# Performance work log

Hardware: AMD Instinct MI355X
Metric: run time of the kernel (lower is better)

The kernel has to match this reference:

```python
import jax, jax.numpy as jnp
import numpy as np

T, B_SZ = 1024, 1024
NX, NU, ND, NM, NDT, NH = 128, 64, 32, 32, 32, 128


def setup_inputs() -> dict:
    key = jax.random.key(0)
    ks = jax.random.split(key, 10)
    return {
        "x": jax.random.normal(ks[0], (B_SZ, NX), jnp.float32),
        "M_flow": jax.random.normal(ks[1], (T, B_SZ, NM), jnp.float32),
        "DT": jax.random.normal(ks[2], (T, B_SZ, NDT), jnp.float32),
        "D": jax.random.normal(ks[3], (T, B_SZ, ND), jnp.float32),
        # ConstrainedLinear(nx, nx): weight and scalar init with torch.rand -> uniform[0,1)
        "A_weight": jax.random.uniform(ks[4], (NX, NX), jnp.float32),
        "A_scalar": jax.random.uniform(ks[5], (NX, NX), jnp.float32),
        # nn.Linear(in, out, bias=False) weights are [out, in]
        "B_w": jax.random.normal(ks[6], (NX, NU), jnp.float32) * (1.0 / np.sqrt(NU)),
        "E_w": jax.random.normal(ks[7], (NX, ND), jnp.float32) * (1.0 / np.sqrt(ND)),
        "hf1_w": jax.random.normal(ks[8], (NH, NM + NDT), jnp.float32) * (1.0 / np.sqrt(NM + NDT)),
        "hf2_w": jax.random.normal(ks[9], (NU, NH), jnp.float32) * (1.0 / np.sqrt(NH)),
    }


def reference(x, M_flow, DT, D, A_weight, A_scalar, B_w, E_w, hf1_w, hf2_w):
    # Constrained weight: ((1 - 0.1*sigmoid(scalar)) * softmax(weight, dim=1)).T
    # It is constant across time, so compute once (torch redundantly recomputes it per step).
    s_clamped = 1.0 - 0.1 * jax.nn.sigmoid(A_scalar)
    W_eff = (s_clamped * jax.nn.softmax(A_weight, axis=1)).T  # [nx, nx]

    # Per-step control input u_t depends only on exogenous M_flow/DT -> vectorize over time.
    md = jnp.concatenate([M_flow, DT], axis=2)                # [T, B, n_m+n_dT]
    h = jax.nn.relu(jnp.einsum('tbi,hi->tbh', md, hf1_w))     # [T, B, n_hidden]
    u = jax.nn.relu(jnp.einsum('tbh,uh->tbu', h, hf2_w))      # [T, B, nu]

    # Precompute additive drive B(u_t) + E(d_t); only x@W_eff is sequential.
    drive = jnp.einsum('tbu,xu->tbx', u, B_w) + jnp.einsum('tbd,xd->tbx', D, E_w)

    def step(x_prev, drive_t):
        x_new = x_prev @ W_eff + drive_t
        return x_new, x_new

    _, X = jax.lax.scan(step, x, drive)  # X: [T, B, nx]
    Y = X[:, :, -1]                      # [T, B]
    return X, Y
```

## Files before the change

kernel.cpp:

```cpp
#include <hip/hip_runtime.h>

typedef _Float16 h4 __attribute__((ext_vector_type(4)));
typedef _Float16 h8 __attribute__((ext_vector_type(8)));
typedef float f4 __attribute__((ext_vector_type(4)));

#define MFMA16(a, b, c) __builtin_amdgcn_mfma_f32_16x16x32_f16((a), (b), (c), 0, 0, 0)

static constexpr int TT  = 1024;
static constexpr int BS  = 1024;
static constexpr int LCH = 64;
static constexpr int NCH = 16;
static constexpr size_t XTOT = (size_t)TT * BS * 128;

static constexpr size_t WS_WT16 = 0;
static constexpr size_t WS_HF1  = 32768;
static constexpr size_t WS_HF2  = 49152;
static constexpr size_t WS_BW   = 65536;
static constexpr size_t WS_EW   = 81920;
static constexpr size_t WS_W32A = 122880;
static constexpr size_t WS_W32B = 188416;
static constexpr size_t WS_F    = 253952;
static constexpr size_t WS_INIT = WS_F + (size_t)NCH * BS * 128 * 4;
static constexpr size_t WS_DRV  = WS_INIT + (size_t)NCH * BS * 128 * 4;

__global__ void prep_kernel(const float* __restrict__ Aw, const float* __restrict__ As,
                            const float* __restrict__ hf1, const float* __restrict__ hf2,
                            const float* __restrict__ Bw, const float* __restrict__ Ew,
                            char* __restrict__ ws)
{
    const int tid = threadIdx.x;
    const int bid = blockIdx.x;
    if (bid < 128) {
        __shared__ float red[128];
        const int n = bid;
        const float a = Aw[n * 128 + tid];
        red[tid] = a;
        __syncthreads();
        for (int s = 64; s > 0; s >>= 1) {
            if (tid < s) red[tid] = fmaxf(red[tid], red[tid + s]);
            __syncthreads();
        }
        const float mx = red[0];
        __syncthreads();
        const float e = expf(a - mx);
        red[tid] = e;
        __syncthreads();
        for (int s = 64; s > 0; s >>= 1) {
            if (tid < s) red[tid] += red[tid + s];
            __syncthreads();
        }
        const float sm  = e / red[0];
        const float asv = As[n * 128 + tid];
        const float sc  = 1.0f - 0.1f * (1.0f / (1.0f + expf(-asv)));
        const float val = sc * sm;
        ((_Float16*)(ws + WS_WT16))[n * 128 + tid] = (_Float16)val;
        ((float*)(ws + WS_W32A))[n * 128 + tid]    = val;
    } else {
        const int b2 = bid - 128;
        for (int i = b2 * 128 + tid; i < 8192; i += 32 * 128) {
            ((_Float16*)(ws + WS_HF1))[i] = (_Float16)hf1[i];
            ((_Float16*)(ws + WS_HF2))[i] = (_Float16)hf2[i];
            ((_Float16*)(ws + WS_BW))[i]  = (_Float16)Bw[i];
            if (i < 4096) ((_Float16*)(ws + WS_EW))[i] = (_Float16)Ew[i];
        }
    }
}

__global__ void matsq_kernel(const float* __restrict__ in, float* __restrict__ out)
{
    const int idx = blockIdx.x * 256 + threadIdx.x;
    const int n = idx >> 7, k = idx & 127;
    float acc = 0.f;
    for (int m = 0; m < 128; ++m) acc += in[m * 128 + k] * in[n * 128 + m];
    out[idx] = acc;
}

__global__ __launch_bounds__(256, 3)
void drive_kernel(const float* __restrict__ Mfl, const float* __restrict__ DTi,
                  const float* __restrict__ Din, char* __restrict__ ws)
{
    const int tid  = threadIdx.x;
    const int lane = tid & 63;
    const int w    = tid >> 6;
    const int cl   = lane & 15;
    const int gq   = lane >> 4;
    const int bt   = blockIdx.x & 63;
    const int tq   = blockIdx.x >> 6;
    const int b0   = bt * 16;

    const _Float16* Hf1  = (const _Float16*)(ws + WS_HF1);
    const _Float16* Hf2  = (const _Float16*)(ws + WS_HF2);
    const _Float16* Bw16 = (const _Float16*)(ws + WS_BW);
    const _Float16* Ew16 = (const _Float16*)(ws + WS_EW);
    _Float16* Drv        = (_Float16*)(ws + WS_DRV);

    __shared__ __align__(16) _Float16 mds[4][16 * 64];
    __shared__ __align__(16) _Float16 dts[4][16 * 32];
    __shared__ __align__(16) _Float16 hs[4][16 * 128];
    __shared__ __align__(16) _Float16 us[4][16 * 64];

    h8 hf1f[2][2], bwf[2][2], ewf[2], hf2f[4];
#pragma unroll
    for (int nt = 0; nt < 2; ++nt) {
        const int ng = w * 32 + nt * 16 + cl;
#pragma unroll
        for (int kk = 0; kk < 2; ++kk) {
            hf1f[nt][kk] = *(const h8*)&Hf1[ng * 64 + kk * 32 + gq * 8];
            bwf[nt][kk]  = *(const h8*)&Bw16[ng * 64 + kk * 32 + gq * 8];
        }
        ewf[nt] = *(const h8*)&Ew16[ng * 32 + gq * 8];
    }
    {
        const int ng = w * 16 + cl;
#pragma unroll
        for (int kk = 0; kk < 4; ++kk)
            hf2f[kk] = *(const h8*)&Hf2[ng * 128 + kk * 32 + gq * 8];
    }

    const int qrow = (tid & 127) >> 3;
    const int qc4  = (tid & 7) * 4;
    f4 pm[4], pd[4];
#pragma unroll
    for (int s = 0; s < 4; ++s) {
        const size_t t  = (size_t)tq * 4 + s;
        const size_t rb = (t * BS + b0 + qrow) * 32 + qc4;
        pm[s] = (tid < 128) ? *(const f4*)&Mfl[rb] : *(const f4*)&DTi[rb];
        if (tid < 128) pd[s] = *(const f4*)&Din[rb];
    }
#pragma unroll
    for (int s = 0; s < 4; ++s) {
        const int col = (tid < 128) ? qc4 : (32 + qc4);
        h4 hv;
#pragma unroll
        for (int j = 0; j < 4; ++j) hv[j] = (_Float16)pm[s][j];
        *(h4*)&mds[s][qrow * 64 + (((col >> 3) ^ (qrow & 7)) * 8) + (col & 7)] = hv;
        if (tid < 128) {
            h4 h2;
#pragma unroll
            for (int j = 0; j < 4; ++j) h2[j] = (_Float16)pd[s][j];
            *(h4*)&dts[s][qrow * 32 + (((qc4 >> 3) ^ (qrow & 3)) * 8) + (qc4 & 7)] = h2;
        }
    }
    __syncthreads();

#pragma unroll
    for (int s = 0; s < 4; ++s) {
        f4 ha[2] = {};
#pragma unroll
        for (int kk = 0; kk < 2; ++kk) {
            h8 a = *(const h8*)&mds[s][cl * 64 + (((kk * 4 + gq) ^ (cl & 7)) * 8)];
            ha[0] = MFMA16(a, hf1f[0][kk], ha[0]);
            ha[1] = MFMA16(a, hf1f[1][kk], ha[1]);
        }
#pragma unroll
        for (int nt = 0; nt < 2; ++nt) {
            const int colg = w * 32 + nt * 16 + cl;
#pragma unroll
            for (int r = 0; r < 4; ++r) {
                const int row = gq * 4 + r;
                hs[s][row * 128 + (((colg >> 3) ^ (row & 15)) * 8) + (colg & 7)] =
                    (_Float16)fmaxf(ha[nt][r], 0.f);
            }
        }
    }
    __syncthreads();

#pragma unroll
    for (int s = 0; s < 4; ++s) {
        f4 ua = {};
#pragma unroll
        for (int kk = 0; kk < 4; ++kk) {
            h8 a = *(const h8*)&hs[s][cl * 128 + (((kk * 4 + gq) ^ (cl & 15)) * 8)];
            ua = MFMA16(a, hf2f[kk], ua);
        }
        const int colg = w * 16 + cl;
#pragma unroll
        for (int r = 0; r < 4; ++r) {
            const int row = gq * 4 + r;
            us[s][row * 64 + (((colg >> 3) ^ (row & 7)) * 8) + (colg & 7)] =
                (_Float16)fmaxf(ua[r], 0.f);
        }
    }
    __syncthreads();

#pragma unroll
    for (int s = 0; s < 4; ++s) {
        f4 acc[2] = {};
#pragma unroll
        for (int kk = 0; kk < 2; ++kk) {
            h8 a = *(const h8*)&us[s][cl * 64 + (((kk * 4 + gq) ^ (cl & 7)) * 8)];
            acc[0] = MFMA16(a, bwf[0][kk], acc[0]);
            acc[1] = MFMA16(a, bwf[1][kk], acc[1]);
        }
        {
            h8 a = *(const h8*)&dts[s][cl * 32 + ((gq ^ (cl & 3)) * 8)];
            acc[0] = MFMA16(a, ewf[0], acc[0]);
            acc[1] = MFMA16(a, ewf[1], acc[1]);
        }
        h8 hv;
#pragma unroll
        for (int nt = 0; nt < 2; ++nt)
#pragma unroll
            for (int r = 0; r < 4; ++r) hv[nt * 4 + r] = (_Float16)acc[nt][r];
        const size_t t = (size_t)tq * 4 + s;
        *(h8*)&Drv[((t * 64 + bt) * 256 + tid) * 8] = hv;
    }
}

template <bool FINAL>
__global__ __launch_bounds__(256, 4)
void scan_kernel(char* __restrict__ ws, float* __restrict__ Xout, float* __restrict__ Yout)
{
    const int tid  = threadIdx.x;
    const int lane = tid & 63;
    const int w    = tid >> 6;
    const int cl   = lane & 15;
    const int gq   = lane >> 4;
    const int bt   = blockIdx.x & 63;
    const int c    = blockIdx.x >> 6;
    const int b0   = bt * 16;

    const _Float16* Wt16 = (const _Float16*)(ws + WS_WT16);
    const _Float16* Drv  = (const _Float16*)(ws + WS_DRV);
    float* Fbuf          = (float*)(ws + WS_F);
    const float* Init    = (const float*)(ws + WS_INIT);

    __shared__ __align__(16) _Float16 xs[2][16 * 128];

    h8 wtf[2][4];
#pragma unroll
    for (int nt = 0; nt < 2; ++nt) {
        const int ng = w * 32 + nt * 16 + cl;
#pragma unroll
        for (int kk = 0; kk < 4; ++kk)
            wtf[nt][kk] = *(const h8*)&Wt16[ng * 128 + kk * 32 + gq * 8];
    }

    if constexpr (FINAL) {
        const int row = tid >> 4, c8 = tid & 15;
        const float* src = &Init[((size_t)c * BS + b0 + row) * 128 + c8 * 8];
        f4 v0 = *(const f4*)src;
        f4 v1 = *(const f4*)(src + 4);
        h8 hv;
#pragma unroll
        for (int j = 0; j < 4; ++j) { hv[j] = (_Float16)v0[j]; hv[4 + j] = (_Float16)v1[j]; }
        *(h8*)&xs[0][row * 128 + ((c8 ^ row) & 15) * 8] = hv;
    } else {
        h8 z = {};
        *(h8*)&xs[0][tid * 8] = z;
    }
    __syncthreads();

    const size_t dbase = (((size_t)c * 64) * 64 + bt) * 2048 + (size_t)tid * 8;
    h8 dc = *(const h8*)&Drv[dbase];

    int cur = 0;
    for (int k = 0; k < LCH; ++k) {
        f4 acc[2];
#pragma unroll
        for (int nt = 0; nt < 2; ++nt)
#pragma unroll
            for (int r = 0; r < 4; ++r) acc[nt][r] = (float)dc[nt * 4 + r];

        if (k + 1 < LCH) dc = *(const h8*)&Drv[dbase + (size_t)(k + 1) * 64 * 2048];

#pragma unroll
        for (int kk = 0; kk < 4; ++kk) {
            h8 a = *(const h8*)&xs[cur][cl * 128 + (((kk * 4 + gq) ^ (cl & 15)) * 8)];
            acc[0] = MFMA16(a, wtf[0][kk], acc[0]);
            acc[1] = MFMA16(a, wtf[1][kk], acc[1]);
        }

        const int nxt = cur ^ 1;
        if constexpr (FINAL) {
            const size_t t = (size_t)c * LCH + k;
#pragma unroll
            for (int nt = 0; nt < 2; ++nt) {
                const int colg = w * 32 + nt * 16 + cl;
#pragma unroll
                for (int r = 0; r < 4; ++r) {
                    const int row = gq * 4 + r;
                    const float v = acc[nt][r];
                    Xout[(t * BS + b0 + row) * 128 + colg] = v;
                    xs[nxt][row * 128 + (((colg >> 3) ^ (row & 15)) * 8) + (colg & 7)] =
                        (_Float16)v;
                }
            }
            if (w == 3 && cl == 15) {
#pragma unroll
                for (int r = 0; r < 4; ++r)
                    Yout[t * BS + b0 + gq * 4 + r] = acc[1][r];
            }
        } else {
            if (k == LCH - 1) {
#pragma unroll
                for (int nt = 0; nt < 2; ++nt) {
                    const int colg = w * 32 + nt * 16 + cl;
#pragma unroll
                    for (int r = 0; r < 4; ++r) {
                        const int row = gq * 4 + r;
                        Fbuf[((size_t)c * BS + b0 + row) * 128 + colg] = acc[nt][r];
                    }
                }
            } else {
#pragma unroll
                for (int nt = 0; nt < 2; ++nt) {
                    const int colg = w * 32 + nt * 16 + cl;
#pragma unroll
                    for (int r = 0; r < 4; ++r) {
                        const int row = gq * 4 + r;
                        xs[nxt][row * 128 + (((colg >> 3) ^ (row & 15)) * 8) + (colg & 7)] =
                            (_Float16)acc[nt][r];
                    }
                }
            }
        }
        __syncthreads();
        cur = nxt;
    }
}

__global__ __launch_bounds__(256, 2)
void carry_kernel(const float* __restrict__ x_in, char* __restrict__ ws)
{
    const int tid  = threadIdx.x;
    const int lane = tid & 63;
    const int w    = tid >> 6;
    const int cl   = lane & 15;
    const int gq   = lane >> 4;
    const int b0   = blockIdx.x * 16;

    const float* WL32 = (const float*)(ws + WS_W32A);
    const float* Fbuf = (const float*)(ws + WS_F);
    float* Init       = (float*)(ws + WS_INIT);

    __shared__ __align__(16) _Float16 xs[2][16 * 128];

    h8 wlf[2][4];
#pragma unroll
    for (int nt = 0; nt < 2; ++nt) {
        const int ng = w * 32 + nt * 16 + cl;
#pragma unroll
        for (int kk = 0; kk < 4; ++kk) {
            f4 a0 = *(const f4*)&WL32[ng * 128 + kk * 32 + gq * 8];
            f4 a1 = *(const f4*)&WL32[ng * 128 + kk * 32 + gq * 8 + 4];
#pragma unroll
            for (int j = 0; j < 4; ++j) {
                wlf[nt][kk][j]     = (_Float16)a0[j];
                wlf[nt][kk][4 + j] = (_Float16)a1[j];
            }
        }
    }

    {
        const int row = tid >> 4, c8 = tid & 15;
        const float* src = &x_in[(b0 + row) * 128 + c8 * 8];
        f4 v0 = *(const f4*)src, v1 = *(const f4*)(src + 4);
        float* dst = &Init[((size_t)(b0 + row)) * 128 + c8 * 8];
        *(f4*)dst = v0;
        *(f4*)(dst + 4) = v1;
        h8 hv;
#pragma unroll
        for (int j = 0; j < 4; ++j) { hv[j] = (_Float16)v0[j]; hv[4 + j] = (_Float16)v1[j]; }
        *(h8*)&xs[0][row * 128 + ((c8 ^ row) & 15) * 8] = hv;
    }
    __syncthreads();

    int cur = 0;
    for (int cc = 1; cc < NCH; ++cc) {
        f4 acc[2] = {};
#pragma unroll
        for (int kk = 0; kk < 4; ++kk) {
            h8 a = *(const h8*)&xs[cur][cl * 128 + (((kk * 4 + gq) ^ (cl & 15)) * 8)];
            acc[0] = MFMA16(a, wlf[0][kk], acc[0]);
            acc[1] = MFMA16(a, wlf[1][kk], acc[1]);
        }
        const int nxt = cur ^ 1;
#pragma unroll
        for (int nt = 0; nt < 2; ++nt) {
            const int colg = w * 32 + nt * 16 + cl;
#pragma unroll
            for (int r = 0; r < 4; ++r) {
                const int row = gq * 4 + r;
                const float v =
                    acc[nt][r] + Fbuf[((size_t)(cc - 1) * BS + b0 + row) * 128 + colg];
                Init[((size_t)cc * BS + b0 + row) * 128 + colg] = v;
                xs[nxt][row * 128 + (((colg >> 3) ^ (row & 15)) * 8) + (colg & 7)] =
                    (_Float16)v;
            }
        }
        __syncthreads();
        cur = nxt;
    }
}

extern "C" void kernel_launch(void* const* d_in, const int* in_sizes, int n_in,
                              void* d_out, int out_size, void* d_ws, size_t ws_size,
                              hipStream_t stream)
{
    const float* x_in = (const float*)d_in[0];
    const float* Mfl  = (const float*)d_in[1];
    const float* DTi  = (const float*)d_in[2];
    const float* Din  = (const float*)d_in[3];
    const float* Aw   = (const float*)d_in[4];
    const float* As   = (const float*)d_in[5];
    const float* Bw   = (const float*)d_in[6];
    const float* Ew   = (const float*)d_in[7];
    const float* hf1  = (const float*)d_in[8];
    const float* hf2  = (const float*)d_in[9];
    char* ws    = (char*)d_ws;
    float* Xout = (float*)d_out;
    float* Yout = Xout + XTOT;

    prep_kernel<<<dim3(160), dim3(128), 0, stream>>>(Aw, As, hf1, hf2, Bw, Ew, ws);

    float* A32 = (float*)(ws + WS_W32A);
    float* B32 = (float*)(ws + WS_W32B);
    for (int i = 0; i < 6; ++i) {
        const float* src = (i & 1) ? B32 : A32;
        float* dst       = (i & 1) ? A32 : B32;
        matsq_kernel<<<dim3(64), dim3(256), 0, stream>>>(src, dst);
    }

    drive_kernel<<<dim3(256 * 64), dim3(256), 0, stream>>>(Mfl, DTi, Din, ws);

    scan_kernel<false><<<dim3(15 * 64), dim3(256), 0, stream>>>(ws, nullptr, nullptr);
    carry_kernel<<<dim3(64), dim3(256), 0, stream>>>(x_in, ws);
    scan_kernel<true><<<dim3(16 * 64), dim3(256), 0, stream>>>(ws, Xout, Yout);
}
```

Baseline: 457.5 us.

## Split pipeline into two halves, compute W^64 with MFMA, add nontemporal I/O

The 1024 time steps are now processed in two halves of 512. Each half runs drive, chunk scan, carry and final scan, so the drive buffer only holds 8 chunks and is reused between halves. The six fp32 matrix-squaring launches are replaced by a single-block fp16 MFMA kernel that builds W^64 in shared memory. Inputs are read and outputs written with nontemporal hints, and the per-step drive prefetch is double-buffered two steps ahead. W^64 now carries fp16 rounding at each squaring, which may reduce accuracy of the carried chunk states, and the split adds launches and serialization between halves.

Measured after the change: 435.0 us. 1.05x faster.

```diff
diff --git a/kernel.cpp b/kernel.cpp
--- a/kernel.cpp
+++ b/kernel.cpp
@@ -17,11 +17,13 @@
 static constexpr size_t WS_HF2  = 49152;
 static constexpr size_t WS_BW   = 65536;
 static constexpr size_t WS_EW   = 81920;
-static constexpr size_t WS_W32A = 122880;
-static constexpr size_t WS_W32B = 188416;
+static constexpr size_t WS_W64  = 122880;
 static constexpr size_t WS_F    = 253952;
 static constexpr size_t WS_INIT = WS_F + (size_t)NCH * BS * 128 * 4;
 static constexpr size_t WS_DRV  = WS_INIT + (size_t)NCH * BS * 128 * 4;
+
+template <typename T>
+__device__ inline T ntload(const T* p) { return __builtin_nontemporal_load(p); }
 
 __global__ void prep_kernel(const float* __restrict__ Aw, const float* __restrict__ As,
                             const float* __restrict__ hf1, const float* __restrict__ hf2,
@@ -52,9 +54,7 @@
         const float sm  = e / red[0];
         const float asv = As[n * 128 + tid];
         const float sc  = 1.0f - 0.1f * (1.0f / (1.0f + expf(-asv)));
-        const float val = sc * sm;
-        ((_Float16*)(ws + WS_WT16))[n * 128 + tid] = (_Float16)val;
-        ((float*)(ws + WS_W32A))[n * 128 + tid]    = val;
+        ((_Float16*)(ws + WS_WT16))[n * 128 + tid] = (_Float16)(sc * sm);
     } else {
         const int b2 = bid - 128;
         for (int i = b2 * 128 + tid; i < 8192; i += 32 * 128) {
@@ -66,18 +66,65 @@
     }
 }
 
-__global__ void matsq_kernel(const float* __restrict__ in, float* __restrict__ out)
-{
-    const int idx = blockIdx.x * 256 + threadIdx.x;
-    const int n = idx >> 7, k = idx & 127;
-    float acc = 0.f;
-    for (int m = 0; m < 128; ++m) acc += in[m * 128 + k] * in[n * 128 + m];
-    out[idx] = acc;
-}
-
-__global__ __launch_bounds__(256, 3)
+__global__ void w64_kernel(char* __restrict__ ws)
+{
+    const int tid  = threadIdx.x;
+    const int lane = tid & 63;
+    const int w    = tid >> 6;
+    const int cl   = lane & 15;
+    const int gq   = lane >> 4;
+
+    __shared__ __align__(16) _Float16 Ta[128 * 128];
+    __shared__ __align__(16) _Float16 Tb[128 * 128];
+
+    const _Float16* Wt16 = (const _Float16*)(ws + WS_WT16);
+    for (int i = tid; i < 2048; i += 256)
+        *(h8*)&Ta[i * 8] = *(const h8*)&Wt16[i * 8];
+    __syncthreads();
+
+    for (int s = 0; s < 6; ++s) {
+        const _Float16* src = (s & 1) ? Tb : Ta;
+        _Float16* dst       = (s & 1) ? Ta : Tb;
+        f4 acc[8][2];
+#pragma unroll
+        for (int mt = 0; mt < 8; ++mt)
+#pragma unroll
+            for (int nt = 0; nt < 2; ++nt) acc[mt][nt] = f4{};
+#pragma unroll
+        for (int kk = 0; kk < 4; ++kk) {
+            h8 b0, b1;
+#pragma unroll
+            for (int j = 0; j < 8; ++j) {
+                const int kr = kk * 32 + gq * 8 + j;
+                b0[j] = src[kr * 128 + w * 32 + cl];
+                b1[j] = src[kr * 128 + w * 32 + 16 + cl];
+            }
+#pragma unroll
+            for (int mt = 0; mt < 8; ++mt) {
+                h8 a = *(const h8*)&src[(mt * 16 + cl) * 128 + kk * 32 + gq * 8];
+                acc[mt][0] = MFMA16(a, b0, acc[mt][0]);
+                acc[mt][1] = MFMA16(a, b1, acc[mt][1]);
+            }
+        }
+        __syncthreads();
+#pragma unroll
+        for (int mt = 0; mt < 8; ++mt)
+#pragma unroll
+            for (int nt = 0; nt < 2; ++nt)
+#pragma unroll
+                for (int r = 0; r < 4; ++r)
+                    dst[(mt * 16 + gq * 4 + r) * 128 + w * 32 + nt * 16 + cl] =
+                        (_Float16)acc[mt][nt][r];
+        __syncthreads();
+    }
+    _Float16* W64 = (_Float16*)(ws + WS_W64);
+    for (int i = tid; i < 2048; i += 256)
+        *(h8*)&W64[i * 8] = *(const h8*)&Ta[i * 8];
+}
+
+__global__ __launch_bounds__(256, 4)
 void drive_kernel(const float* __restrict__ Mfl, const float* __restrict__ DTi,
-                  const float* __restrict__ Din, char* __restrict__ ws)
+                  const float* __restrict__ Din, char* __restrict__ ws, int t0)
 {
     const int tid  = threadIdx.x;
     const int lane = tid & 63;
@@ -99,33 +146,15 @@
     __shared__ __align__(16) _Float16 hs[4][16 * 128];
     __shared__ __align__(16) _Float16 us[4][16 * 64];
 
-    h8 hf1f[2][2], bwf[2][2], ewf[2], hf2f[4];
-#pragma unroll
-    for (int nt = 0; nt < 2; ++nt) {
-        const int ng = w * 32 + nt * 16 + cl;
-#pragma unroll
-        for (int kk = 0; kk < 2; ++kk) {
-            hf1f[nt][kk] = *(const h8*)&Hf1[ng * 64 + kk * 32 + gq * 8];
-            bwf[nt][kk]  = *(const h8*)&Bw16[ng * 64 + kk * 32 + gq * 8];
-        }
-        ewf[nt] = *(const h8*)&Ew16[ng * 32 + gq * 8];
-    }
-    {
-        const int ng = w * 16 + cl;
-#pragma unroll
-        for (int kk = 0; kk < 4; ++kk)
-            hf2f[kk] = *(const h8*)&Hf2[ng * 128 + kk * 32 + gq * 8];
-    }
-
     const int qrow = (tid & 127) >> 3;
     const int qc4  = (tid & 7) * 4;
     f4 pm[4], pd[4];
 #pragma unroll
     for (int s = 0; s < 4; ++s) {
-        const size_t t  = (size_t)tq * 4 + s;
+        const size_t t  = (size_t)(t0 + tq * 4 + s);
         const size_t rb = (t * BS + b0 + qrow) * 32 + qc4;
-        pm[s] = (tid < 128) ? *(const f4*)&Mfl[rb] : *(const f4*)&DTi[rb];
-        if (tid < 128) pd[s] = *(const f4*)&Din[rb];
+        pm[s] = (tid < 128) ? ntload((const f4*)&Mfl[rb]) : ntload((const f4*)&DTi[rb]);
+        if (tid < 128) pd[s] = ntload((const f4*)&Din[rb]);
     }
 #pragma unroll
     for (int s = 0; s < 4; ++s) {
@@ -141,6 +170,24 @@
             *(h4*)&dts[s][qrow * 32 + (((qc4 >> 3) ^ (qrow & 3)) * 8) + (qc4 & 7)] = h2;
         }
     }
+
+    h8 hf1f[2][2], bwf[2][2], ewf[2], hf2f[4];
+#pragma unroll
+    for (int nt = 0; nt < 2; ++nt) {
+        const int ng = w * 32 + nt * 16 + cl;
+#pragma unroll
+        for (int kk = 0; kk < 2; ++kk) {
+            hf1f[nt][kk] = *(const h8*)&Hf1[ng * 64 + kk * 32 + gq * 8];
+            bwf[nt][kk]  = *(const h8*)&Bw16[ng * 64 + kk * 32 + gq * 8];
+        }
+        ewf[nt] = *(const h8*)&Ew16[ng * 32 + gq * 8];
+    }
+    {
+        const int ng = w * 16 + cl;
+#pragma unroll
+        for (int kk = 0; kk < 4; ++kk)
+            hf2f[kk] = *(const h8*)&Hf2[ng * 128 + kk * 32 + gq * 8];
+    }
     __syncthreads();
 
 #pragma unroll
@@ -202,14 +249,15 @@
         for (int nt = 0; nt < 2; ++nt)
 #pragma unroll
             for (int r = 0; r < 4; ++r) hv[nt * 4 + r] = (_Float16)acc[nt][r];
-        const size_t t = (size_t)tq * 4 + s;
-        *(h8*)&Drv[((t * 64 + bt) * 256 + tid) * 8] = hv;
+        const size_t tl = (size_t)tq * 4 + s;
+        *(h8*)&Drv[((tl * 64 + bt) * 256 + tid) * 8] = hv;
     }
 }
 
 template <bool FINAL>
 __global__ __launch_bounds__(256, 4)
-void scan_kernel(char* __restrict__ ws, float* __restrict__ Xout, float* __restrict__ Yout)
+void scan_kernel(char* __restrict__ ws, int c0, float* __restrict__ Xout,
+                 float* __restrict__ Yout)
 {
     const int tid  = threadIdx.x;
     const int lane = tid & 63;
@@ -217,7 +265,8 @@
     const int cl   = lane & 15;
     const int gq   = lane >> 4;
     const int bt   = blockIdx.x & 63;
-    const int c    = blockIdx.x >> 6;
+    const int cg   = c0 + (blockIdx.x >> 6);
+    const int cloc = cg & 7;
     const int b0   = bt * 16;
 
     const _Float16* Wt16 = (const _Float16*)(ws + WS_WT16);
@@ -238,7 +287,7 @@
 
     if constexpr (FINAL) {
         const int row = tid >> 4, c8 = tid & 15;
-        const float* src = &Init[((size_t)c * BS + b0 + row) * 128 + c8 * 8];
+        const float* src = &Init[((size_t)cg * BS + b0 + row) * 128 + c8 * 8];
         f4 v0 = *(const f4*)src;
         f4 v1 = *(const f4*)(src + 4);
         h8 hv;
@@ -251,18 +300,16 @@
     }
     __syncthreads();
 
-    const size_t dbase = (((size_t)c * 64) * 64 + bt) * 2048 + (size_t)tid * 8;
-    h8 dc = *(const h8*)&Drv[dbase];
+    const size_t doff = (size_t)cloc * 64 * 131072 + (size_t)bt * 2048 + (size_t)tid * 8;
+    auto LD = [&](int k) -> h8 { return *(const h8*)&Drv[doff + (size_t)k * 131072]; };
 
     int cur = 0;
-    for (int k = 0; k < LCH; ++k) {
+    auto step = [&](int k, const h8& dc) {
         f4 acc[2];
 #pragma unroll
         for (int nt = 0; nt < 2; ++nt)
 #pragma unroll
             for (int r = 0; r < 4; ++r) acc[nt][r] = (float)dc[nt * 4 + r];
-
-        if (k + 1 < LCH) dc = *(const h8*)&Drv[dbase + (size_t)(k + 1) * 64 * 2048];
 
 #pragma unroll
         for (int kk = 0; kk < 4; ++kk) {
@@ -273,7 +320,7 @@
 
         const int nxt = cur ^ 1;
         if constexpr (FINAL) {
-            const size_t t = (size_t)c * LCH + k;
+            const size_t t = (size_t)cg * LCH + k;
 #pragma unroll
             for (int nt = 0; nt < 2; ++nt) {
                 const int colg = w * 32 + nt * 16 + cl;
@@ -281,7 +328,7 @@
                 for (int r = 0; r < 4; ++r) {
                     const int row = gq * 4 + r;
                     const float v = acc[nt][r];
-                    Xout[(t * BS + b0 + row) * 128 + colg] = v;
+                    __builtin_nontemporal_store(v, &Xout[(t * BS + b0 + row) * 128 + colg]);
                     xs[nxt][row * 128 + (((colg >> 3) ^ (row & 15)) * 8) + (colg & 7)] =
                         (_Float16)v;
                 }
@@ -289,7 +336,7 @@
             if (w == 3 && cl == 15) {
 #pragma unroll
                 for (int r = 0; r < 4; ++r)
-                    Yout[t * BS + b0 + gq * 4 + r] = acc[1][r];
+                    __builtin_nontemporal_store(acc[1][r], &Yout[t * BS + b0 + gq * 4 + r]);
             }
         } else {
             if (k == LCH - 1) {
@@ -299,7 +346,7 @@
 #pragma unroll
                     for (int r = 0; r < 4; ++r) {
                         const int row = gq * 4 + r;
-                        Fbuf[((size_t)c * BS + b0 + row) * 128 + colg] = acc[nt][r];
+                        Fbuf[((size_t)cg * BS + b0 + row) * 128 + colg] = acc[nt][r];
                     }
                 }
             } else {
@@ -317,11 +364,27 @@
         }
         __syncthreads();
         cur = nxt;
+    };
+
+    h8 dc0 = LD(0);
+    h8 dc1 = LD(1);
+    for (int k = 0; k < LCH; k += 2) {
+        {
+            h8 d = dc0;
+            if (k + 2 < LCH) dc0 = LD(k + 2);
+            step(k, d);
+        }
+        {
+            h8 d = dc1;
+            if (k + 3 < LCH) dc1 = LD(k + 3);
+            step(k + 1, d);
+        }
     }
 }
 
 __global__ __launch_bounds__(256, 2)
-void carry_kernel(const float* __restrict__ x_in, char* __restrict__ ws)
+void carry_kernel(const float* __restrict__ x0, char* __restrict__ ws,
+                  int cc_lo, int cc_hi, int copy0)
 {
     const int tid  = threadIdx.x;
     const int lane = tid & 63;
@@ -330,9 +393,9 @@
     const int gq   = lane >> 4;
     const int b0   = blockIdx.x * 16;
 
-    const float* WL32 = (const float*)(ws + WS_W32A);
-    const float* Fbuf = (const float*)(ws + WS_F);
-    float* Init       = (float*)(ws + WS_INIT);
+    const _Float16* W64 = (const _Float16*)(ws + WS_W64);
+    const float* Fbuf   = (const float*)(ws + WS_F);
+    float* Init         = (float*)(ws + WS_INIT);
 
     __shared__ __align__(16) _Float16 xs[2][16 * 128];
 
@@ -341,24 +404,19 @@
     for (int nt = 0; nt < 2; ++nt) {
         const int ng = w * 32 + nt * 16 + cl;
 #pragma unroll
-        for (int kk = 0; kk < 4; ++kk) {
-            f4 a0 = *(const f4*)&WL32[ng * 128 + kk * 32 + gq * 8];
-            f4 a1 = *(const f4*)&WL32[ng * 128 + kk * 32 + gq * 8 + 4];
-#pragma unroll
-            for (int j = 0; j < 4; ++j) {
-                wlf[nt][kk][j]     = (_Float16)a0[j];
-                wlf[nt][kk][4 + j] = (_Float16)a1[j];
-            }
-        }
+        for (int kk = 0; kk < 4; ++kk)
+            wlf[nt][kk] = *(const h8*)&W64[ng * 128 + kk * 32 + gq * 8];
     }
 
     {
         const int row = tid >> 4, c8 = tid & 15;
-        const float* src = &x_in[(b0 + row) * 128 + c8 * 8];
+        const float* src = &x0[(b0 + row) * 128 + c8 * 8];
         f4 v0 = *(const f4*)src, v1 = *(const f4*)(src + 4);
-        float* dst = &Init[((size_t)(b0 + row)) * 128 + c8 * 8];
-        *(f4*)dst = v0;
-        *(f4*)(dst + 4) = v1;
+        if (copy0) {
+            float* dst = &Init[((size_t)cc_lo * BS + b0 + row) * 128 + c8 * 8];
+            *(f4*)dst = v0;
+            *(f4*)(dst + 4) = v1;
+        }
         h8 hv;
 #pragma unroll
         for (int j = 0; j < 4; ++j) { hv[j] = (_Float16)v0[j]; hv[4 + j] = (_Float16)v1[j]; }
@@ -367,7 +425,7 @@
     __syncthreads();
 
     int cur = 0;
-    for (int cc = 1; cc < NCH; ++cc) {
+    for (int cc = cc_lo + 1; cc <= cc_hi; ++cc) {
         f4 acc[2] = {};
 #pragma unroll
         for (int kk = 0; kk < 4; ++kk) {
@@ -411,20 +469,18 @@
     char* ws    = (char*)d_ws;
     float* Xout = (float*)d_out;
     float* Yout = Xout + XTOT;
+    const float* Init8 = (const float*)(ws + WS_INIT) + (size_t)8 * BS * 128;
 
     prep_kernel<<<dim3(160), dim3(128), 0, stream>>>(Aw, As, hf1, hf2, Bw, Ew, ws);
-
-    float* A32 = (float*)(ws + WS_W32A);
-    float* B32 = (float*)(ws + WS_W32B);
-    for (int i = 0; i < 6; ++i) {
-        const float* src = (i & 1) ? B32 : A32;
-        float* dst       = (i & 1) ? A32 : B32;
-        matsq_kernel<<<dim3(64), dim3(256), 0, stream>>>(src, dst);
-    }
-
-    drive_kernel<<<dim3(256 * 64), dim3(256), 0, stream>>>(Mfl, DTi, Din, ws);
-
-    scan_kernel<false><<<dim3(15 * 64), dim3(256), 0, stream>>>(ws, nullptr, nullptr);
-    carry_kernel<<<dim3(64), dim3(256), 0, stream>>>(x_in, ws);
-    scan_kernel<true><<<dim3(16 * 64), dim3(256), 0, stream>>>(ws, Xout, Yout);
-}
+    w64_kernel<<<dim3(1), dim3(256), 0, stream>>>(ws);
+
+    drive_kernel<<<dim3(128 * 64), dim3(256), 0, stream>>>(Mfl, DTi, Din, ws, 0);
+    scan_kernel<false><<<dim3(8 * 64), dim3(256), 0, stream>>>(ws, 0, nullptr, nullptr);
+    carry_kernel<<<dim3(64), dim3(256), 0, stream>>>(x_in, ws, 0, 8, 1);
+    scan_kernel<true><<<dim3(8 * 64), dim3(256), 0, stream>>>(ws, 0, Xout, Yout);
+
+    drive_kernel<<<dim3(128 * 64), dim3(256), 0, stream>>>(Mfl, DTi, Din, ws, 512);
+    scan_kernel<false><<<dim3(7 * 64), dim3(256), 0, stream>>>(ws, 8, nullptr, nullptr);
+    carry_kernel<<<dim3(64), dim3(256), 0, stream>>>(Init8, ws, 8, 15, 0);
+    scan_kernel<true><<<dim3(8 * 64), dim3(256), 0, stream>>>(ws, 8, Xout, Yout);
+}
```
